# Optimization experiments

Measured on AMD Instinct MI355X. Metric: run time of the kernel, lower is better.

The kernel has to match this reference:

```python
import jax, jax.numpy as jnp
import numpy as np

H = 4096          # hidden_size
NH = 32           # num query heads
NKV = 8           # num kv heads
HD = H // NH      # head_dim = 128
GROUPS = NH // NKV
ROPE_BASE = 100000.0
B, S = 1, 2048


def setup_inputs() -> dict:
    key = jax.random.key(0)
    k1, k2, k3 = jax.random.split(key, 3)
    hidden_states = jax.random.normal(k1, (B, S, H), dtype=jnp.float32)
    position_ids = jnp.broadcast_to(jnp.arange(S, dtype=jnp.int32), (B, S))
    op_size = NH * HD + 2 * NKV * HD  # 6144
    w_qkv = jax.random.normal(k2, (op_size, H), dtype=jnp.float32) * 0.02
    w_o = jax.random.normal(k3, (H, H), dtype=jnp.float32) * 0.02
    return {"hidden_states": hidden_states, "position_ids": position_ids,
            "w_qkv": w_qkv, "w_o": w_o}


def _rotate_half(x):
    x1, x2 = x[..., : HD // 2], x[..., HD // 2 :]
    return jnp.concatenate((-x2, x1), axis=-1)


def _rope_cos_sin(position_ids, dtype):
    # inv_freq: [HD/2]
    inv_freq = 1.0 / (ROPE_BASE ** (jnp.arange(0, HD, 2, dtype=jnp.float32) / HD))
    freqs = position_ids.astype(jnp.float32)[..., None] * inv_freq  # [B,S,HD/2]
    emb = jnp.concatenate((freqs, freqs), axis=-1)                  # [B,S,HD]
    return jnp.cos(emb).astype(dtype), jnp.sin(emb).astype(dtype)


def reference(hidden_states, position_ids, w_qkv, w_o):
    b, s, _ = hidden_states.shape
    qkv = jnp.einsum('bsh,oh->bso', hidden_states, w_qkv)
    q_end = NH * HD
    k_end = q_end + NKV * HD
    q = qkv[..., :q_end].reshape(b, s, NH, HD)
    k = qkv[..., q_end:k_end].reshape(b, s, NKV, HD)
    v = qkv[..., k_end:].reshape(b, s, NKV, HD)

    cos, sin = _rope_cos_sin(position_ids, hidden_states.dtype)  # [B,S,HD]
    cos, sin = cos[:, :, None, :], sin[:, :, None, :]            # broadcast over heads
    q = q * cos + _rotate_half(q) * sin
    k = k * cos + _rotate_half(k) * sin

    # GQA: repeat kv heads
    k = jnp.repeat(k, GROUPS, axis=2)  # [B,S,NH,HD]
    v = jnp.repeat(v, GROUPS, axis=2)

    scale = 1.0 / jnp.sqrt(jnp.asarray(HD, dtype=q.dtype))
    scores = jnp.einsum('bqhd,bkhd->bhqk', q, k) * scale  # [B,NH,S,S]
    causal = jnp.tril(jnp.ones((s, s), dtype=bool))
    scores = jnp.where(causal[None, None], scores, jnp.finfo(scores.dtype).min)
    probs = jax.nn.softmax(scores, axis=-1)
    attn = jnp.einsum('bhqk,bkhd->bqhd', probs, v).reshape(b, s, H)
    return jnp.einsum('bsh,oh->bso', attn, w_o)
```

## Files before the change

kernel.cpp:

```cpp
#include <hip/hip_runtime.h>

#define SEQ     2048
#define HDIM    4096
#define NHEADS  32
#define NKVH    8
#define HEADD   128
#define QKV_LD  6144
#define K_OFF   4096
#define V_OFF   5120

typedef __bf16 bf16x8 __attribute__((ext_vector_type(8)));
typedef float  f32x4  __attribute__((ext_vector_type(4)));

__device__ inline float bf2f(unsigned short u) {
  return __uint_as_float(((unsigned int)u) << 16);
}
__device__ inline unsigned short f2bf(float f) {
  unsigned int u = __float_as_uint(f);
  u += 0x7fff + ((u >> 16) & 1);
  return (unsigned short)(u >> 16);
}
__device__ inline unsigned int pack2bf(float a, float b) {
  return (unsigned int)f2bf(a) | ((unsigned int)f2bf(b) << 16);
}

__global__ __launch_bounds__(256) void cvt_all(
    const float* __restrict__ s0, const float* __restrict__ s1,
    const float* __restrict__ s2, unsigned short* __restrict__ d,
    int n0_8, int n1_8, int n2_8) {
  const int total = n0_8 + n1_8 + n2_8;
  for (int i = blockIdx.x * 256 + threadIdx.x; i < total; i += gridDim.x * 256) {
    const float* s; int off;
    if (i < n0_8)              { s = s0; off = i; }
    else if (i < n0_8 + n1_8)  { s = s1; off = i - n0_8; }
    else                       { s = s2; off = i - n0_8 - n1_8; }
    const float* p = s + (size_t)off * 8;
    float4 x = *(const float4*)p;
    float4 y = *(const float4*)(p + 4);
    uint4 pk;
    pk.x = pack2bf(x.x, x.y);
    pk.y = pack2bf(x.z, x.w);
    pk.z = pack2bf(y.x, y.y);
    pk.w = pack2bf(y.z, y.w);
    *(uint4*)(d + (size_t)i * 8) = pk;
  }
}

template<int A_BF16, int B_BF16, int C_F32>
__global__ __launch_bounds__(256, 2) void gemm_bt(
    const void* __restrict__ Av,
    const void* __restrict__ Bv,
    void* __restrict__ Cv,
    int K, int lda, int ldb, int ldc) {
  __shared__ __align__(16) unsigned short sA[128][64];
  __shared__ __align__(16) unsigned short sB[128][64];

  const int t    = threadIdx.x;
  const int wave = t >> 6;
  const int lane = t & 63;
  const int lrow = lane & 15;
  const int kgrp = lane >> 4;
  const int wm   = (wave >> 1) * 64;
  const int wn   = (wave & 1) * 64;
  const int m0   = blockIdx.x * 128;
  const int n0   = blockIdx.y * 128;

  f32x4 acc[4][4];
  #pragma unroll
  for (int i = 0; i < 4; ++i)
    #pragma unroll
    for (int j = 0; j < 4; ++j)
      #pragma unroll
      for (int e = 0; e < 4; ++e) acc[i][j][e] = 0.f;

  for (int k0 = 0; k0 < K; k0 += 64) {
    __syncthreads();
    if constexpr (A_BF16) {
      #pragma unroll
      for (int c = 0; c < 4; ++c) {
        int chunk = wave * 4 + c;
        int row   = chunk * 8 + (lane >> 3);
        int cg    = (lane & 7) ^ ((lane >> 3) & 7);
        __builtin_amdgcn_global_load_lds(
            (const __attribute__((address_space(1))) unsigned int*)
                ((const unsigned short*)Av + (size_t)(m0 + row) * lda + k0 + cg * 8),
            (__attribute__((address_space(3))) unsigned int*)&sA[chunk * 8][0],
            16, 0, 0);
      }
    } else {
      #pragma unroll
      for (int r = 0; r < 4; ++r) {
        int row = r * 32 + (t >> 3);
        int cg  = t & 7;
        const float* p = (const float*)Av + (size_t)(m0 + row) * lda + k0 + cg * 8;
        float4 x = *(const float4*)p;
        float4 y = *(const float4*)(p + 4);
        uint4 pk;
        pk.x = pack2bf(x.x, x.y);
        pk.y = pack2bf(x.z, x.w);
        pk.z = pack2bf(y.x, y.y);
        pk.w = pack2bf(y.z, y.w);
        *(uint4*)&sA[row][(cg ^ (row & 7)) * 8] = pk;
      }
    }
    if constexpr (B_BF16) {
      #pragma unroll
      for (int c = 0; c < 4; ++c) {
        int chunk = wave * 4 + c;
        int row   = chunk * 8 + (lane >> 3);
        int cg    = (lane & 7) ^ ((lane >> 3) & 7);
        __builtin_amdgcn_global_load_lds(
            (const __attribute__((address_space(1))) unsigned int*)
                ((const unsigned short*)Bv + (size_t)(n0 + row) * ldb + k0 + cg * 8),
            (__attribute__((address_space(3))) unsigned int*)&sB[chunk * 8][0],
            16, 0, 0);
      }
    } else {
      #pragma unroll
      for (int r = 0; r < 4; ++r) {
        int row = r * 32 + (t >> 3);
        int cg  = t & 7;
        const float* p = (const float*)Bv + (size_t)(n0 + row) * ldb + k0 + cg * 8;
        float4 x = *(const float4*)p;
        float4 y = *(const float4*)(p + 4);
        uint4 pk;
        pk.x = pack2bf(x.x, x.y);
        pk.y = pack2bf(x.z, x.w);
        pk.z = pack2bf(y.x, y.y);
        pk.w = pack2bf(y.z, y.w);
        *(uint4*)&sB[row][(cg ^ (row & 7)) * 8] = pk;
      }
    }
    __syncthreads();

    #pragma unroll
    for (int ks = 0; ks < 2; ++ks) {
      bf16x8 af[4], bfm[4];
      #pragma unroll
      for (int i = 0; i < 4; ++i)
        af[i] = *(const bf16x8*)&sA[wm + i*16 + lrow][((ks*4 + kgrp) ^ (lrow & 7)) * 8];
      #pragma unroll
      for (int j = 0; j < 4; ++j)
        bfm[j] = *(const bf16x8*)&sB[wn + j*16 + lrow][((ks*4 + kgrp) ^ (lrow & 7)) * 8];
      #pragma unroll
      for (int i = 0; i < 4; ++i)
        #pragma unroll
        for (int j = 0; j < 4; ++j)
          acc[i][j] = __builtin_amdgcn_mfma_f32_16x16x32_bf16(af[i], bfm[j], acc[i][j], 0, 0, 0);
    }
  }

  #pragma unroll
  for (int i = 0; i < 4; ++i) {
    #pragma unroll
    for (int r = 0; r < 4; ++r) {
      int row = m0 + wm + i*16 + kgrp*4 + r;
      #pragma unroll
      for (int j = 0; j < 4; ++j) {
        int col = n0 + wn + j*16 + lrow;
        if constexpr (C_F32)
          ((float*)Cv)[(size_t)row * ldc + col] = acc[i][j][r];
        else
          ((unsigned short*)Cv)[(size_t)row * ldc + col] = f2bf(acc[i][j][r]);
      }
    }
  }
}

__global__ __launch_bounds__(256) void rope_transpose(
    unsigned short* __restrict__ qkv, const int* __restrict__ pos,
    unsigned short* __restrict__ vT) {
  __shared__ unsigned short tile[64][72];
  int b = blockIdx.x;
  if (b < 512) {
    int tid = b * 256 + threadIdx.x;
    int d   = tid & 63;
    int s   = tid >> 6;
    float inv = __expf((float)d * -0.17988946039016608f);
    float ang = (float)pos[s] * inv;
    float sn, c;
    sincosf(ang, &sn, &c);
    unsigned short* base = qkv + (size_t)s * QKV_LD + d;
    #pragma unroll 4
    for (int head = 0; head < 40; ++head) {
      unsigned short* p = base + head * 128;
      float x1 = bf2f(p[0]);
      float x2 = bf2f(p[64]);
      p[0]  = f2bf(x1 * c - x2 * sn);
      p[64] = f2bf(x2 * c + x1 * sn);
    }
  } else {
    b -= 512;
    const int t  = threadIdx.x;
    const int s0 = (b & 31) * 64;
    const int c0 = (b >> 5) * 64;
    const int r  = t >> 3;
    const int cg = (t & 7) * 8;
    #pragma unroll
    for (int rr = 0; rr < 2; ++rr) {
      int row = rr * 32 + r;
      *(uint4*)&tile[row][cg] =
          *(const uint4*)(qkv + (size_t)(s0 + row) * QKV_LD + V_OFF + c0 + cg);
    }
    __syncthreads();
    #pragma unroll
    for (int rr = 0; rr < 2; ++rr) {
      int c = rr * 32 + r;
      unsigned short v[8];
      #pragma unroll
      for (int j = 0; j < 8; ++j) v[j] = tile[cg + j][c];
      *(uint4*)(vT + (size_t)(c0 + c) * SEQ + s0 + cg) = *(uint4*)v;
    }
  }
}

__device__ inline bf16x8 scale_frag(bf16x8 v, float s) {
  bf16x8 r;
  #pragma unroll
  for (int j = 0; j < 8; ++j) r[j] = (__bf16)((float)v[j] * s);
  return r;
}

__device__ __forceinline__ void qk_softmax_tile(
    const bf16x8* qf, const unsigned short (*sK)[128],
    unsigned short (*sP)[72],
    f32x4* of, float* m_i, float* l_i,
    int lane, int wave, int dq, bool diag) {
  const int lrow = lane & 15;
  const int kgrp = lane >> 4;
  f32x4 st[4];
  #pragma unroll
  for (int tn = 0; tn < 4; ++tn)
    #pragma unroll
    for (int e = 0; e < 4; ++e) st[tn][e] = 0.f;
  #pragma unroll
  for (int ks = 0; ks < 4; ++ks) {
    #pragma unroll
    for (int tn = 0; tn < 4; ++tn) {
      int cgr = ks * 4 + kgrp;
      const bf16x8 kb = *(const bf16x8*)
          &sK[tn*16 + lrow][((cgr & 8) | ((cgr & 7) ^ (lrow & 7))) * 8];
      st[tn] = __builtin_amdgcn_mfma_f32_16x16x32_bf16(qf[ks], kb, st[tn], 0, 0, 0);
    }
  }
  float mrow[4] = {-1e30f, -1e30f, -1e30f, -1e30f};
  if (diag) {
    #pragma unroll
    for (int tn = 0; tn < 4; ++tn)
      #pragma unroll
      for (int r = 0; r < 4; ++r) {
        float s = st[tn][r];
        if (tn*16 + lrow > dq + r) s = -1e30f;
        st[tn][r] = s;
        mrow[r] = fmaxf(mrow[r], s);
      }
  } else {
    #pragma unroll
    for (int tn = 0; tn < 4; ++tn)
      #pragma unroll
      for (int r = 0; r < 4; ++r)
        mrow[r] = fmaxf(mrow[r], st[tn][r]);
  }
  #pragma unroll
  for (int r = 0; r < 4; ++r)
    #pragma unroll
    for (int off = 1; off < 16; off <<= 1)
      mrow[r] = fmaxf(mrow[r], __shfl_xor(mrow[r], off, 16));
  float alpha[4];
  #pragma unroll
  for (int r = 0; r < 4; ++r) {
    float mnew = fmaxf(m_i[r], mrow[r]);
    alpha[r] = exp2f(m_i[r] - mnew);
    m_i[r] = mnew;
  }
  float rsum[4] = {0.f, 0.f, 0.f, 0.f};
  #pragma unroll
  for (int tn = 0; tn < 4; ++tn)
    #pragma unroll
    for (int r = 0; r < 4; ++r) {
      float pr = exp2f(st[tn][r] - m_i[r]);
      rsum[r] += pr;
      sP[wave*16 + kgrp*4 + r][tn*16 + lrow] = f2bf(pr);
    }
  #pragma unroll
  for (int r = 0; r < 4; ++r) {
    #pragma unroll
    for (int off = 1; off < 16; off <<= 1)
      rsum[r] += __shfl_xor(rsum[r], off, 16);
    l_i[r] = l_i[r] * alpha[r] + rsum[r];
  }
  #pragma unroll
  for (int tt = 0; tt < 8; ++tt)
    #pragma unroll
    for (int r = 0; r < 4; ++r)
      of[tt][r] *= alpha[r];
}

__device__ __forceinline__ void pv_tile(
    const unsigned short (*sP)[72], const unsigned short (*sVt)[64],
    f32x4* of, int lane, int wave) {
  const int lrow = lane & 15;
  const int kgrp = lane >> 4;
  #pragma unroll
  for (int ks = 0; ks < 2; ++ks) {
    const bf16x8 pa = *(const bf16x8*)&sP[wave*16 + lrow][ks*32 + kgrp*8];
    #pragma unroll
    for (int tt = 0; tt < 8; ++tt) {
      int cgr = ks * 4 + kgrp;
      const bf16x8 vb = *(const bf16x8*)
          &sVt[tt*16 + lrow][(cgr ^ (lrow & 7)) * 8];
      of[tt] = __builtin_amdgcn_mfma_f32_16x16x32_bf16(pa, vb, of[tt], 0, 0, 0);
    }
  }
}

__global__ __launch_bounds__(256, 2) void attn_fwd2(
    unsigned short* __restrict__ qkv, const unsigned short* __restrict__ vT) {
  __shared__ __align__(16) unsigned short sK[64][128];
  __shared__ __align__(16) unsigned short sVt[128][64];
  __shared__ __align__(16) unsigned short sP[128][72];

  const int t    = threadIdx.x;
  const int wave = t >> 6;
  const int lane = t & 63;
  const int lrow = lane & 15;
  const int kgrp = lane >> 4;
  const int p    = blockIdx.x;
  const int h    = blockIdx.y;
  const int kvh  = h >> 2;
  const int qLo  = p * 64;
  const int qHi  = (31 - p) * 64;
  const int nTiles = 32 - p;
  const int nDual  = p + 1;

  const float scale2 = 0.12751743f;
  bf16x8 qfH[4], qfL[4];
  {
    const unsigned short* qr =
        qkv + (size_t)(qHi + wave*16 + lrow) * QKV_LD + h * HEADD;
    #pragma unroll
    for (int ks = 0; ks < 4; ++ks)
      qfH[ks] = scale_frag(*(const bf16x8*)(qr + ks*32 + kgrp*8), scale2);
    qr = qkv + (size_t)(qLo + wave*16 + lrow) * QKV_LD + h * HEADD;
    #pragma unroll
    for (int ks = 0; ks < 4; ++ks)
      qfL[ks] = scale_frag(*(const bf16x8*)(qr + ks*32 + kgrp*8), scale2);
  }

  f32x4 ofH[8], ofL[8];
  float mH[4], lH[4], mL[4], lL[4];
  #pragma unroll
  for (int tt = 0; tt < 8; ++tt)
    #pragma unroll
    for (int e = 0; e < 4; ++e) { ofH[tt][e] = 0.f; ofL[tt][e] = 0.f; }
  #pragma unroll
  for (int r = 0; r < 4; ++r) { mH[r] = -1e30f; lH[r] = 0.f; mL[r] = -1e30f; lL[r] = 0.f; }

  for (int kt = 0; kt < nTiles; ++kt) {
    const int k0 = kt * 64;
    __syncthreads();
    #pragma unroll
    for (int c = 0; c < 4; ++c) {
      int cc   = wave * 4 + c;
      int grow = cc * 4 + (lane >> 4);
      int slot = lane & 15;
      int cg   = (slot & 8) | ((slot & 7) ^ (grow & 7));
      __builtin_amdgcn_global_load_lds(
          (const __attribute__((address_space(1))) unsigned int*)
              (qkv + (size_t)(k0 + grow) * QKV_LD + K_OFF + kvh*HEADD + cg*8),
          (__attribute__((address_space(3))) unsigned int*)&sK[cc*4][0],
          16, 0, 0);
    }
    #pragma unroll
    for (int c = 0; c < 4; ++c) {
      int cc   = wave * 4 + c;
      int grow = cc * 8 + (lane >> 3);
      int slot = lane & 7;
      int cg   = slot ^ (grow & 7);
      __builtin_amdgcn_global_load_lds(
          (const __attribute__((address_space(1))) unsigned int*)
              (vT + (size_t)(kvh*HEADD + grow) * SEQ + k0 + cg*8),
          (__attribute__((address_space(3))) unsigned int*)&sVt[cc*8][0],
          16, 0, 0);
    }
    __syncthreads();

    const bool dual = (kt < nDual);
    qk_softmax_tile(qfH, sK, &sP[0],  ofH, mH, lH, lane, wave,
                    qHi + wave*16 + kgrp*4 - k0, k0 == qHi);
    if (dual)
      qk_softmax_tile(qfL, sK, &sP[64], ofL, mL, lL, lane, wave,
                      qLo + wave*16 + kgrp*4 - k0, k0 == qLo);
    __syncthreads();
    pv_tile(&sP[0], sVt, ofH, lane, wave);
    if (dual) pv_tile(&sP[64], sVt, ofL, lane, wave);
  }

  #pragma unroll
  for (int r = 0; r < 4; ++r) {
    float invH = 1.f / lH[r];
    float invL = 1.f / lL[r];
    int rowH = qHi + wave*16 + kgrp*4 + r;
    int rowL = qLo + wave*16 + kgrp*4 + r;
    #pragma unroll
    for (int tt = 0; tt < 8; ++tt) {
      qkv[(size_t)rowH * QKV_LD + h*HEADD + tt*16 + lrow] = f2bf(ofH[tt][r] * invH);
      qkv[(size_t)rowL * QKV_LD + h*HEADD + tt*16 + lrow] = f2bf(ofL[tt][r] * invL);
    }
  }
}

__global__ __launch_bounds__(256) void rope_kernel(
    unsigned short* __restrict__ qkv, const int* __restrict__ pos) {
  int tid  = blockIdx.x * 256 + threadIdx.x;
  int d    = tid & 63;
  int s    = tid >> 6;
  if (s >= SEQ) return;
  float inv = __expf((float)d * -0.17988946039016608f);
  float ang = (float)pos[s] * inv;
  float sn, c;
  sincosf(ang, &sn, &c);
  unsigned short* base = qkv + (size_t)s * QKV_LD + d;
  #pragma unroll 4
  for (int head = 0; head < 40; ++head) {
    unsigned short* p = base + head * 128;
    float x1 = bf2f(p[0]);
    float x2 = bf2f(p[64]);
    p[0]  = f2bf(x1 * c - x2 * sn);
    p[64] = f2bf(x2 * c + x1 * sn);
  }
}

__global__ __launch_bounds__(256, 2) void attn_fwd(
    unsigned short* __restrict__ qkv) {
  __shared__ __align__(16) unsigned short sK[64][136];
  __shared__ __align__(16) unsigned short sVt[128][72];
  __shared__ __align__(16) unsigned short sP[64][72];

  const int t    = threadIdx.x;
  const int wave = t >> 6;
  const int lane = t & 63;
  const int lrow = lane & 15;
  const int kgrp = lane >> 4;
  const int q0   = blockIdx.x * 64;
  const int h    = blockIdx.y;
  const int kvh  = h >> 2;

  bf16x8 qf[4];
  {
    const unsigned short* qrow =
        qkv + (size_t)(q0 + wave*16 + lrow) * QKV_LD + h * HEADD;
    #pragma unroll
    for (int ks = 0; ks < 4; ++ks)
      qf[ks] = *(const bf16x8*)(qrow + ks*32 + kgrp*8);
  }

  f32x4 of[8];
  #pragma unroll
  for (int tt = 0; tt < 8; ++tt)
    #pragma unroll
    for (int e = 0; e < 4; ++e) of[tt][e] = 0.f;
  float m_i[4], l_i[4];
  #pragma unroll
  for (int r = 0; r < 4; ++r) { m_i[r] = -1e30f; l_i[r] = 0.f; }

  const float scale = 0.08838834764831845f;

  for (int k0 = 0; k0 <= q0; k0 += 64) {
    __syncthreads();
    {
      int krow = t >> 4;
      int kcol = (t & 15) * 8;
      #pragma unroll
      for (int r = 0; r < 4; ++r)
        *(uint4*)&sK[r*16 + krow][kcol] =
            *(const uint4*)(qkv + (size_t)(k0 + r*16 + krow) * QKV_LD + K_OFF + kvh*HEADD + kcol);
      int vrow = t & 15;
      int vcol = (t >> 4) * 8;
      #pragma unroll
      for (int r = 0; r < 4; ++r) {
        uint4 v = *(const uint4*)(qkv + (size_t)(k0 + r*16 + vrow) * QKV_LD + V_OFF + kvh*HEADD + vcol);
        const unsigned short* pv = (const unsigned short*)&v;
        #pragma unroll
        for (int j = 0; j < 8; ++j)
          sVt[vcol + j][r*16 + vrow] = pv[j];
      }
    }
    __syncthreads();

    f32x4 st[4];
    #pragma unroll
    for (int tn = 0; tn < 4; ++tn)
      #pragma unroll
      for (int e = 0; e < 4; ++e) st[tn][e] = 0.f;
    #pragma unroll
    for (int ks = 0; ks < 4; ++ks)
      #pragma unroll
      for (int tn = 0; tn < 4; ++tn) {
        bf16x8 kb = *(const bf16x8*)&sK[tn*16 + lrow][ks*32 + kgrp*8];
        st[tn] = __builtin_amdgcn_mfma_f32_16x16x32_bf16(qf[ks], kb, st[tn], 0, 0, 0);
      }

    float mrow[4];
    #pragma unroll
    for (int r = 0; r < 4; ++r) mrow[r] = -1e30f;
    const int qrow_base = q0 + wave*16 + kgrp*4;
    #pragma unroll
    for (int tn = 0; tn < 4; ++tn) {
      int kcol = k0 + tn*16 + lrow;
      #pragma unroll
      for (int r = 0; r < 4; ++r) {
        float s = st[tn][r] * scale;
        if (kcol > qrow_base + r) s = -1e30f;
        st[tn][r] = s;
        mrow[r] = fmaxf(mrow[r], s);
      }
    }
    #pragma unroll
    for (int r = 0; r < 4; ++r)
      #pragma unroll
      for (int off = 1; off < 16; off <<= 1)
        mrow[r] = fmaxf(mrow[r], __shfl_xor(mrow[r], off, 16));

    float alpha[4];
    #pragma unroll
    for (int r = 0; r < 4; ++r) {
      float mnew = fmaxf(m_i[r], mrow[r]);
      alpha[r] = __expf(m_i[r] - mnew);
      m_i[r] = mnew;
    }

    float rsum[4] = {0.f, 0.f, 0.f, 0.f};
    #pragma unroll
    for (int tn = 0; tn < 4; ++tn)
      #pragma unroll
      for (int r = 0; r < 4; ++r) {
        float pr = __expf(st[tn][r] - m_i[r]);
        rsum[r] += pr;
        sP[wave*16 + kgrp*4 + r][tn*16 + lrow] = f2bf(pr);
      }
    #pragma unroll
    for (int r = 0; r < 4; ++r) {
      #pragma unroll
      for (int off = 1; off < 16; off <<= 1)
        rsum[r] += __shfl_xor(rsum[r], off, 16);
      l_i[r] = l_i[r] * alpha[r] + rsum[r];
    }
    #pragma unroll
    for (int tt = 0; tt < 8; ++tt)
      #pragma unroll
      for (int r = 0; r < 4; ++r)
        of[tt][r] *= alpha[r];

    __syncthreads();

    #pragma unroll
    for (int ks = 0; ks < 2; ++ks) {
      bf16x8 pa = *(const bf16x8*)&sP[wave*16 + lrow][ks*32 + kgrp*8];
      #pragma unroll
      for (int tt = 0; tt < 8; ++tt) {
        bf16x8 vb = *(const bf16x8*)&sVt[tt*16 + lrow][ks*32 + kgrp*8];
        of[tt] = __builtin_amdgcn_mfma_f32_16x16x32_bf16(pa, vb, of[tt], 0, 0, 0);
      }
    }
  }

  #pragma unroll
  for (int r = 0; r < 4; ++r) {
    int row = q0 + wave*16 + kgrp*4 + r;
    float inv = 1.f / l_i[r];
    #pragma unroll
    for (int tt = 0; tt < 8; ++tt)
      qkv[(size_t)row * QKV_LD + h*HEADD + tt*16 + lrow] = f2bf(of[tt][r] * inv);
  }
}

extern "C" void kernel_launch(void* const* d_in, const int* in_sizes, int n_in,
                              void* d_out, int out_size, void* d_ws, size_t ws_size,
                              hipStream_t stream) {
  const float* hs    = (const float*)d_in[0];
  const int*   pos   = (const int*)d_in[1];
  const float* w_qkv = (const float*)d_in[2];
  const float* w_o   = (const float*)d_in[3];
  float*       out   = (float*)d_out;

  const size_t N_QKV  = (size_t)SEQ * QKV_LD;
  const size_t N_HS   = (size_t)SEQ * HDIM;
  const size_t N_WQKV = (size_t)QKV_LD * HDIM;
  const size_t N_WO   = (size_t)HDIM * HDIM;

  unsigned short* qkv = (unsigned short*)d_ws;

  const size_t full_ws = (N_QKV + N_HS + N_WQKV + N_WO) * 2;

  if (ws_size >= full_ws) {
    unsigned short* hs_b   = qkv + N_QKV;
    unsigned short* wqkv_b = hs_b + N_HS;
    unsigned short* wo_b   = wqkv_b + N_WQKV;
    unsigned short* vT     = hs_b;

    cvt_all<<<2048, 256, 0, stream>>>(hs, w_qkv, w_o, hs_b,
                                      (int)(N_HS / 8), (int)(N_WQKV / 8),
                                      (int)(N_WO / 8));
    gemm_bt<1, 1, 0><<<dim3(SEQ/128, QKV_LD/128), 256, 0, stream>>>(
        hs_b, wqkv_b, qkv, HDIM, HDIM, HDIM, QKV_LD);
    rope_transpose<<<1024, 256, 0, stream>>>(qkv, pos, vT);
    attn_fwd2<<<dim3(16, NHEADS), 256, 0, stream>>>(qkv, vT);
    gemm_bt<1, 1, 1><<<dim3(SEQ/128, HDIM/128), 256, 0, stream>>>(
        qkv, wo_b, out, HDIM, QKV_LD, HDIM, HDIM);
  } else {
    gemm_bt<0, 0, 0><<<dim3(SEQ/128, QKV_LD/128), 256, 0, stream>>>(
        hs, w_qkv, qkv, HDIM, HDIM, HDIM, QKV_LD);
    rope_kernel<<<SEQ * 64 / 256, 256, 0, stream>>>(qkv, pos);
    attn_fwd<<<dim3(SEQ/64, NHEADS), 256, 0, stream>>>(qkv);
    gemm_bt<1, 0, 1><<<dim3(SEQ/128, HDIM/128), 256, 0, stream>>>(
        qkv, w_o, out, HDIM, QKV_LD, HDIM, HDIM);
  }
}
```

Baseline: 529.2 us.

## Double-buffer K/V tiles in attention and drop the mid-loop barrier

Splits the K and V^T shared-memory tiles into two buffers. The next tile's async global-to-LDS load is issued right after the loop-top barrier, so it overlaps the QK/softmax/PV work on the current tile. The P scratch shrinks to 64 rows and is reused by the high and low query blocks. Each wave writes and reads only its own P rows, which removes the second __syncthreads per iteration. Separately, converting P to bf16 now truncates instead of rounding to nearest even. This saves ALU work at a small accuracy cost, and the doubled K/V buffers raise LDS use per block.

```diff
diff --git a/kernel.cpp b/kernel.cpp
--- a/kernel.cpp
+++ b/kernel.cpp
@@ -280,7 +280,8 @@
     for (int r = 0; r < 4; ++r) {
       float pr = exp2f(st[tn][r] - m_i[r]);
       rsum[r] += pr;
-      sP[wave*16 + kgrp*4 + r][tn*16 + lrow] = f2bf(pr);
+      sP[wave*16 + kgrp*4 + r][tn*16 + lrow] =
+          (unsigned short)(__float_as_uint(pr) >> 16);
     }
   #pragma unroll
   for (int r = 0; r < 4; ++r) {
@@ -316,9 +317,9 @@
 
 __global__ __launch_bounds__(256, 2) void attn_fwd2(
     unsigned short* __restrict__ qkv, const unsigned short* __restrict__ vT) {
-  __shared__ __align__(16) unsigned short sK[64][128];
-  __shared__ __align__(16) unsigned short sVt[128][64];
-  __shared__ __align__(16) unsigned short sP[128][72];
+  __shared__ __align__(16) unsigned short sK[2][64][128];
+  __shared__ __align__(16) unsigned short sVt[2][128][64];
+  __shared__ __align__(16) unsigned short sP[64][72];
 
   const int t    = threadIdx.x;
   const int wave = t >> 6;
@@ -356,9 +357,7 @@
   #pragma unroll
   for (int r = 0; r < 4; ++r) { mH[r] = -1e30f; lH[r] = 0.f; mL[r] = -1e30f; lL[r] = 0.f; }
 
-  for (int kt = 0; kt < nTiles; ++kt) {
-    const int k0 = kt * 64;
-    __syncthreads();
+  auto stage = [&](int k0, int b) {
     #pragma unroll
     for (int c = 0; c < 4; ++c) {
       int cc   = wave * 4 + c;
@@ -368,32 +367,37 @@
       __builtin_amdgcn_global_load_lds(
           (const __attribute__((address_space(1))) unsigned int*)
               (qkv + (size_t)(k0 + grow) * QKV_LD + K_OFF + kvh*HEADD + cg*8),
-          (__attribute__((address_space(3))) unsigned int*)&sK[cc*4][0],
+          (__attribute__((address_space(3))) unsigned int*)&sK[b][cc*4][0],
           16, 0, 0);
     }
     #pragma unroll
     for (int c = 0; c < 4; ++c) {
       int cc   = wave * 4 + c;
       int grow = cc * 8 + (lane >> 3);
-      int slot = lane & 7;
-      int cg   = slot ^ (grow & 7);
+      int cg   = (lane & 7) ^ (grow & 7);
       __builtin_amdgcn_global_load_lds(
           (const __attribute__((address_space(1))) unsigned int*)
               (vT + (size_t)(kvh*HEADD + grow) * SEQ + k0 + cg*8),
-          (__attribute__((address_space(3))) unsigned int*)&sVt[cc*8][0],
+          (__attribute__((address_space(3))) unsigned int*)&sVt[b][cc*8][0],
           16, 0, 0);
     }
+  };
+
+  stage(0, 0);
+  for (int kt = 0; kt < nTiles; ++kt) {
+    const int k0 = kt * 64;
+    const int b  = kt & 1;
     __syncthreads();
-
-    const bool dual = (kt < nDual);
-    qk_softmax_tile(qfH, sK, &sP[0],  ofH, mH, lH, lane, wave,
+    if (kt + 1 < nTiles) stage(k0 + 64, b ^ 1);
+
+    qk_softmax_tile(qfH, sK[b], sP, ofH, mH, lH, lane, wave,
                     qHi + wave*16 + kgrp*4 - k0, k0 == qHi);
-    if (dual)
-      qk_softmax_tile(qfL, sK, &sP[64], ofL, mL, lL, lane, wave,
+    pv_tile(sP, sVt[b], ofH, lane, wave);
+    if (kt < nDual) {
+      qk_softmax_tile(qfL, sK[b], sP, ofL, mL, lL, lane, wave,
                       qLo + wave*16 + kgrp*4 - k0, k0 == qLo);
-    __syncthreads();
-    pv_tile(&sP[0], sVt, ofH, lane, wave);
-    if (dual) pv_tile(&sP[64], sVt, ofL, lane, wave);
+      pv_tile(sP, sVt[b], ofL, lane, wave);
+    }
   }
 
   #pragma unroll
```

Measured after the change: 552.8 us. +4.5%, slower.
